# Kernel tuning notes

Hardware: AMD Instinct MI355X
Metric: run time of the kernel (lower is better)

Reference implementation:

```python
import jax, jax.numpy as jnp
import numpy as np

VOCAB = 256
H = 4096
N_LAYERS = 2


def setup_inputs() -> dict:
    key = jax.random.key(0)
    ks = jax.random.split(key, 16)
    s = 1.0 / np.sqrt(H)
    inp = jax.random.randint(ks[0], (1,), 0, VOCAB)
    hidden = jax.random.normal(ks[1], (N_LAYERS, 1, H), dtype=jnp.float32)
    emb = jax.random.normal(ks[2], (VOCAB, H), dtype=jnp.float32)
    def u(k, shape):
        return jax.random.uniform(k, shape, jnp.float32, -s, s)
    return {
        'inp': inp,
        'hidden': hidden,
        'emb': emb,
        'W_ih0': u(ks[3], (3 * H, H)), 'W_hh0': u(ks[4], (3 * H, H)),
        'b_ih0': u(ks[5], (3 * H,)),   'b_hh0': u(ks[6], (3 * H,)),
        'W_ih1': u(ks[7], (3 * H, H)), 'W_hh1': u(ks[8], (3 * H, H)),
        'b_ih1': u(ks[9], (3 * H,)),   'b_hh1': u(ks[10], (3 * H,)),
        'W_dec': u(ks[11], (VOCAB, H)), 'b_dec': u(ks[12], (VOCAB,)),
    }


def _gru_cell(x, h, W_ih, W_hh, b_ih, b_hh):
    # x, h: [1, H]; PyTorch GRU gate math (gate order r, z, n)
    gi = x @ W_ih.T + b_ih  # [1, 3H]
    gh = h @ W_hh.T + b_hh  # [1, 3H]
    i_r, i_z, i_n = jnp.split(gi, 3, axis=-1)
    h_r, h_z, h_n = jnp.split(gh, 3, axis=-1)
    r = jax.nn.sigmoid(i_r + h_r)
    z = jax.nn.sigmoid(i_z + h_z)
    n = jnp.tanh(i_n + r * h_n)
    return (1.0 - z) * n + z * h


def reference(inp, hidden, emb, W_ih0, W_hh0, b_ih0, b_hh0,
              W_ih1, W_hh1, b_ih1, b_hh1, W_dec, b_dec):
    x = emb[inp]  # [1, H] embedding lookup (encoder)
    params = ((W_ih0, W_hh0, b_ih0, b_hh0), (W_ih1, W_hh1, b_ih1, b_hh1))
    new_h = []
    for l in range(N_LAYERS):
        h = _gru_cell(x, hidden[l], *params[l])  # [1, H]
        new_h.append(h)
        x = h  # output of layer l feeds layer l+1
    output = x @ W_dec.T + b_dec  # [1, VOCAB]
    return output, jnp.stack(new_h, axis=0)
```

## Files before the change

kernel.cpp:

```cpp
#include <hip/hip_runtime.h>

#define H 4096
#define NVOCAB 256
#define NE 8

__global__ __launch_bounds__(384, 3) void gru_layer_kernel(
    const float* __restrict__ Wih,
    const float* __restrict__ Whh,
    const float* __restrict__ bih,
    const float* __restrict__ bhh,
    const float* __restrict__ xbase,
    const int* __restrict__ inp, int use_inp,
    const float* __restrict__ hprev,
    float* __restrict__ hout)
{
    __shared__ float part[6][NE];
    const int wave = threadIdx.x >> 6;
    const int lane = threadIdx.x & 63;
    const int i0   = blockIdx.x * NE;

    const float* x = xbase + (use_inp ? (size_t)inp[0] * H : 0);
    const int g = (wave < 3) ? wave : (wave - 3);
    const float* W    = (wave < 3) ? Wih : Whh;
    const float* vec  = (wave < 3) ? x   : hprev;
    const float* bias = (wave < 3) ? bih : bhh;

    const float4* xr = reinterpret_cast<const float4*>(vec);
    float4 v[16];
#pragma unroll
    for (int it = 0; it < 16; ++it) v[it] = xr[it * 64 + lane];

    for (int e = 0; e < NE; ++e) {
        const int i = i0 + e;
        const float4* wr =
            reinterpret_cast<const float4*>(W + (size_t)(g * H + i) * H);
        float ax = 0.f, ay = 0.f, az = 0.f, aw = 0.f;
#pragma unroll
        for (int half = 0; half < 2; ++half) {
            float4 w[8];
#pragma unroll
            for (int j = 0; j < 8; ++j)
                w[j] = wr[half * 512 + j * 64 + lane];
#pragma unroll
            for (int j = 0; j < 8; ++j) {
                ax += w[j].x * v[half * 8 + j].x;
                ay += w[j].y * v[half * 8 + j].y;
                az += w[j].z * v[half * 8 + j].z;
                aw += w[j].w * v[half * 8 + j].w;
            }
        }
        float acc = (ax + ay) + (az + aw);
#pragma unroll
        for (int off = 32; off > 0; off >>= 1) acc += __shfl_down(acc, off, 64);
        if (lane == 0) part[wave][e] = acc + bias[g * H + i];
    }
    __syncthreads();

    if (threadIdx.x < NE) {
        const int e = threadIdx.x;
        const int i = i0 + e;
        float ir = part[0][e], iz = part[1][e], inn = part[2][e];
        float hr = part[3][e], hz = part[4][e], hn  = part[5][e];
        float r = 1.f / (1.f + __expf(-(ir + hr)));
        float z = 1.f / (1.f + __expf(-(iz + hz)));
        float n = tanhf(inn + r * hn);
        float h = hprev[i];
        hout[i] = (1.f - z) * n + z * h;
    }
}

__global__ __launch_bounds__(256) void dec_kernel(
    const float* __restrict__ Wdec,
    const float* __restrict__ bdec,
    const float* __restrict__ vec,
    float* __restrict__ out)
{
    const int wave = threadIdx.x >> 6;
    const int lane = threadIdx.x & 63;
    const int row = blockIdx.x * 4 + wave;
    const float4* wr = reinterpret_cast<const float4*>(Wdec + (size_t)row * H);
    const float4* xr = reinterpret_cast<const float4*>(vec);
    float ax = 0.f, ay = 0.f, az = 0.f, aw = 0.f;
#pragma unroll
    for (int q = 0; q < 2; ++q) {
        float4 w[8], xv[8];
#pragma unroll
        for (int j = 0; j < 8; ++j) {
            w[j]  = wr[q * 512 + j * 64 + lane];
            xv[j] = xr[q * 512 + j * 64 + lane];
        }
#pragma unroll
        for (int j = 0; j < 8; ++j) {
            ax += w[j].x * xv[j].x;
            ay += w[j].y * xv[j].y;
            az += w[j].z * xv[j].z;
            aw += w[j].w * xv[j].w;
        }
    }
    float acc = (ax + ay) + (az + aw);
#pragma unroll
    for (int off = 32; off > 0; off >>= 1) acc += __shfl_down(acc, off, 64);
    if (lane == 0) out[row] = acc + bdec[row];
}

extern "C" void kernel_launch(void* const* d_in, const int* in_sizes, int n_in,
                              void* d_out, int out_size, void* d_ws, size_t ws_size,
                              hipStream_t stream) {
    const int*   inp    = (const int*)d_in[0];
    const float* hidden = (const float*)d_in[1];
    const float* emb    = (const float*)d_in[2];
    const float* Wih0   = (const float*)d_in[3];
    const float* Whh0   = (const float*)d_in[4];
    const float* bih0   = (const float*)d_in[5];
    const float* bhh0   = (const float*)d_in[6];
    const float* Wih1   = (const float*)d_in[7];
    const float* Whh1   = (const float*)d_in[8];
    const float* bih1   = (const float*)d_in[9];
    const float* bhh1   = (const float*)d_in[10];
    const float* Wdec   = (const float*)d_in[11];
    const float* bdec   = (const float*)d_in[12];

    float* out = (float*)d_out;
    float* h0o = out + NVOCAB;
    float* h1o = out + NVOCAB + H;

    gru_layer_kernel<<<H / NE, 384, 0, stream>>>(
        Wih0, Whh0, bih0, bhh0, emb, inp, 1, hidden, h0o);
    gru_layer_kernel<<<H / NE, 384, 0, stream>>>(
        Wih1, Whh1, bih1, bhh1, h0o, inp, 0, hidden + H, h1o);
    dec_kernel<<<NVOCAB / 4, 256, 0, stream>>>(Wdec, bdec, h1o, out);
}
```

Measured before the change: 641.1 us.

## Split GRU row dot-products across two waves and stage input vectors in LDS

Each block now uses 768 threads, with two waves per gate matrix, each covering half of the 4096-wide row. The x and h vectors are staged once into shared memory and read from there, instead of every wave holding 16 float4 registers. Partial sums from the two halves are combined and the bias is added in the final gate step. The goal is more memory-level parallelism and lower register pressure for this bandwidth-bound GEMV. The cost is 32KB of LDS per block, which may limit how many blocks fit on a CU, plus an extra barrier.

```diff
diff --git a/kernel.cpp b/kernel.cpp
--- a/kernel.cpp
+++ b/kernel.cpp
@@ -3,8 +3,9 @@
 #define H 4096
 #define NVOCAB 256
 #define NE 8
+#define NTHREADS 768
 
-__global__ __launch_bounds__(384, 3) void gru_layer_kernel(
+__global__ __launch_bounds__(NTHREADS, 6) void gru_layer_kernel(
     const float* __restrict__ Wih,
     const float* __restrict__ Whh,
     const float* __restrict__ bih,
@@ -14,56 +15,64 @@
     const float* __restrict__ hprev,
     float* __restrict__ hout)
 {
-    __shared__ float part[6][NE];
-    const int wave = threadIdx.x >> 6;
-    const int lane = threadIdx.x & 63;
+    __shared__ float4 vlds[2][H / 4];
+    __shared__ float part[6][2][NE];
+
+    const int tid  = threadIdx.x;
+    const int wave = tid >> 6;
+    const int lane = tid & 63;
     const int i0   = blockIdx.x * NE;
 
     const float* x = xbase + (use_inp ? (size_t)inp[0] * H : 0);
-    const int g = (wave < 3) ? wave : (wave - 3);
-    const float* W    = (wave < 3) ? Wih : Whh;
-    const float* vec  = (wave < 3) ? x   : hprev;
-    const float* bias = (wave < 3) ? bih : bhh;
 
-    const float4* xr = reinterpret_cast<const float4*>(vec);
-    float4 v[16];
-#pragma unroll
-    for (int it = 0; it < 16; ++it) v[it] = xr[it * 64 + lane];
+    const float4* xr = reinterpret_cast<const float4*>(x);
+    const float4* hr = reinterpret_cast<const float4*>(hprev);
+    for (int idx = tid; idx < H / 4; idx += NTHREADS) {
+        vlds[0][idx] = xr[idx];
+        vlds[1][idx] = hr[idx];
+    }
+    __syncthreads();
+
+    const int p    = wave >> 1;
+    const int half = wave & 1;
+    const int g    = (p < 3) ? p : p - 3;
+    const float*  W  = (p < 3) ? Wih : Whh;
+    const float4* vl = &vlds[(p < 3) ? 0 : 1][half * 512];
+
+    const float4* wbase = reinterpret_cast<const float4*>(
+        W + (size_t)(g * H + i0) * H) + half * 512;
 
     for (int e = 0; e < NE; ++e) {
-        const int i = i0 + e;
-        const float4* wr =
-            reinterpret_cast<const float4*>(W + (size_t)(g * H + i) * H);
+        const float4* wr = wbase + (size_t)e * (H / 4);
+        float4 w[8];
+#pragma unroll
+        for (int j = 0; j < 8; ++j)
+            w[j] = wr[j * 64 + lane];
         float ax = 0.f, ay = 0.f, az = 0.f, aw = 0.f;
 #pragma unroll
-        for (int half = 0; half < 2; ++half) {
-            float4 w[8];
-#pragma unroll
-            for (int j = 0; j < 8; ++j)
-                w[j] = wr[half * 512 + j * 64 + lane];
-#pragma unroll
-            for (int j = 0; j < 8; ++j) {
-                ax += w[j].x * v[half * 8 + j].x;
-                ay += w[j].y * v[half * 8 + j].y;
-                az += w[j].z * v[half * 8 + j].z;
-                aw += w[j].w * v[half * 8 + j].w;
-            }
+        for (int j = 0; j < 8; ++j) {
+            float4 v = vl[j * 64 + lane];
+            ax += w[j].x * v.x; ay += w[j].y * v.y;
+            az += w[j].z * v.z; aw += w[j].w * v.w;
         }
         float acc = (ax + ay) + (az + aw);
 #pragma unroll
         for (int off = 32; off > 0; off >>= 1) acc += __shfl_down(acc, off, 64);
-        if (lane == 0) part[wave][e] = acc + bias[g * H + i];
+        if (lane == 0) part[p][half][e] = acc;
     }
     __syncthreads();
 
-    if (threadIdx.x < NE) {
-        const int e = threadIdx.x;
-        const int i = i0 + e;
-        float ir = part[0][e], iz = part[1][e], inn = part[2][e];
-        float hr = part[3][e], hz = part[4][e], hn  = part[5][e];
-        float r = 1.f / (1.f + __expf(-(ir + hr)));
+    if (tid < NE) {
+        const int e = tid, i = i0 + e;
+        float ir = part[0][0][e] + part[0][1][e] + bih[0 * H + i];
+        float iz = part[1][0][e] + part[1][1][e] + bih[1 * H + i];
+        float in_= part[2][0][e] + part[2][1][e] + bih[2 * H + i];
+        float hrv= part[3][0][e] + part[3][1][e] + bhh[0 * H + i];
+        float hz = part[4][0][e] + part[4][1][e] + bhh[1 * H + i];
+        float hn = part[5][0][e] + part[5][1][e] + bhh[2 * H + i];
+        float r = 1.f / (1.f + __expf(-(ir + hrv)));
         float z = 1.f / (1.f + __expf(-(iz + hz)));
-        float n = tanhf(inn + r * hn);
+        float n = tanhf(in_ + r * hn);
         float h = hprev[i];
         hout[i] = (1.f - z) * n + z * h;
     }
@@ -124,9 +133,9 @@
     float* h0o = out + NVOCAB;
     float* h1o = out + NVOCAB + H;
 
-    gru_layer_kernel<<<H / NE, 384, 0, stream>>>(
+    gru_layer_kernel<<<H / NE, NTHREADS, 0, stream>>>(
         Wih0, Whh0, bih0, bhh0, emb, inp, 1, hidden, h0o);
-    gru_layer_kernel<<<H / NE, 384, 0, stream>>>(
+    gru_layer_kernel<<<H / NE, NTHREADS, 0, stream>>>(
         Wih1, Whh1, bih1, bhh1, h0o, inp, 0, hidden + H, h1o);
     dec_kernel<<<NVOCAB / 4, 256, 0, stream>>>(Wdec, bdec, h1o, out);
 }
```

After: 638.8 us. No clear change (-0.4%).
